# Kernel tuning notes

Hardware: AMD Instinct MI355X
Metric: run time of the kernel (lower is better)

The kernel has to match this reference:

```python
import jax, jax.numpy as jnp
import numpy as np

E = 8          # num_experts
D = 768        # d_model
H = 3072       # d_hidden
TOP_K = 2


def setup_inputs() -> dict:
    key = jax.random.key(0)
    ks = jax.random.split(key, 8)
    s_in = 1.0 / np.sqrt(D)
    s_h = 1.0 / np.sqrt(H)
    return {
        "hidden_states": jax.random.normal(ks[0], (2, 2048, D), dtype=jnp.float32),
        "gate_w": jax.random.normal(ks[1], (E, D), dtype=jnp.float32) * s_in,
        "gate_b": jnp.zeros((E,), dtype=jnp.float32),
        "w1": jax.random.normal(ks[2], (E, H, D), dtype=jnp.float32) * s_in,  # FMoELinear: [E, out, in]
        "b1": jnp.zeros((E, H), dtype=jnp.float32),
        "w2": jax.random.normal(ks[3], (E, D, H), dtype=jnp.float32) * s_h,
        "b2": jnp.zeros((E, D), dtype=jnp.float32),
        "bias": jnp.zeros((D,), dtype=jnp.float32),
    }


def reference(hidden_states, gate_w, gate_b, w1, b1, w2, b2, bias):
    B, S, d = hidden_states.shape
    x = hidden_states.reshape(-1, d)                      # [T, D]
    T = x.shape[0]
    # NaiveGate: linear gate, top-k, softmax over the top-k logits
    logits = x @ gate_w.T + gate_b                        # [T, E]
    top_val, top_idx = jax.lax.top_k(logits, TOP_K)       # [T, K]
    scores = jax.nn.softmax(top_val, axis=-1)             # [T, K]
    # combine weights: [T, E], score mass scattered to chosen experts
    combine = jnp.zeros((T, E), dtype=x.dtype)
    combine = combine.at[jnp.arange(T)[:, None], top_idx].add(scores)
    # expert MLPs (dense over experts, masked combine keeps routing math exact)
    h = jnp.einsum('td,ehd->teh', x, w1) + b1             # [T, E, H]
    h = jax.nn.gelu(h, approximate=False)                 # torch F.gelu (exact erf)
    y = jnp.einsum('teh,edh->ted', h, w2) + b2            # [T, E, D]
    out = jnp.einsum('te,ted->td', combine, y)            # [T, D]
    return out.reshape(B, S, d), bias
```

## Files before the change

### kernel.cpp

```cpp
#include <hip/hip_runtime.h>
#include <hip/hip_bf16.h>

#define DD 768
#define HH 3072
#define NE 8
#define TOPK 2

#define BK 64
#define CAP 1536
#define NRBMAX (CAP/128)
#define NB1 (HH / 128)
#define NB2 (DD / 128)

typedef __attribute__((ext_vector_type(8))) short short8;
typedef __attribute__((ext_vector_type(4))) float f32x4;

static __device__ __forceinline__ unsigned short f2bf(float v) {
    __hip_bfloat16 b = __float2bfloat16(v);
    return *reinterpret_cast<unsigned short*>(&b);
}

static __device__ __forceinline__ float gelu_f(float v) {
    float s = v * 0.70710678118f;
    float a = fabsf(s);
    float t = __builtin_amdgcn_rcpf(1.f + 0.3275911f * a);
    float poly = t * (0.254829592f + t * (-0.284496736f + t * (1.421413741f +
                 t * (-1.453152027f + t * 1.061405429f))));
    float erfv = 1.f - poly * __expf(-s * s);
    erfv = copysignf(erfv, s);
    return 0.5f * v * (1.f + erfv);
}

static __device__ __forceinline__ void cvt4(const float* __restrict__ src,
                                            unsigned short* __restrict__ dst, size_t j4)
{
    float4 v = *reinterpret_cast<const float4*>(&src[j4 * 4]);
    ushort4 o;
    o.x = f2bf(v.x); o.y = f2bf(v.y); o.z = f2bf(v.z); o.w = f2bf(v.w);
    *reinterpret_cast<ushort4*>(&dst[j4 * 4]) = o;
}

__global__ __launch_bounds__(256) void routecvt_kernel(
    const float* __restrict__ x, const float* __restrict__ gw, const float* __restrict__ gb,
    int* __restrict__ ctrl, int* __restrict__ pos_of, float* __restrict__ wpos,
    unsigned short* __restrict__ Xe, int T, int maxP,
    const float* __restrict__ w1, const float* __restrict__ w2,
    unsigned short* __restrict__ w1b, unsigned short* __restrict__ w2b, size_t nW4)
{
    __shared__ int s_e[32], s_rank[32];
    __shared__ float s_w[32];
    __shared__ int lh[NE], lbase[NE];

    int tid = threadIdx.x;
    int w = tid >> 6, lane = tid & 63;

    if ((int)blockIdx.x * 16 < T) {
        if (tid < NE) lh[tid] = 0;
        __syncthreads();

#pragma unroll
        for (int j = 0; j < 4; ++j) {
            int t = blockIdx.x * 16 + w * 4 + j;
            if (t >= T) break;
            float acc[NE];
#pragma unroll
            for (int e = 0; e < NE; ++e) acc[e] = 0.f;
            const float4* xr = reinterpret_cast<const float4*>(x + (size_t)t * DD);
#pragma unroll
            for (int k = 0; k < 3; ++k) {
                float4 xv = xr[k * 64 + lane];
#pragma unroll
                for (int e = 0; e < NE; ++e) {
                    float4 gv = *reinterpret_cast<const float4*>(&gw[e * DD + (k * 64 + lane) * 4]);
                    acc[e] += xv.x * gv.x + xv.y * gv.y + xv.z * gv.z + xv.w * gv.w;
                }
            }
#pragma unroll
            for (int e = 0; e < NE; ++e) {
                float v = acc[e];
                for (int off = 32; off; off >>= 1) v += __shfl_xor(v, off, 64);
                acc[e] = v;
            }
            if (lane == 0) {
                float lg[NE];
#pragma unroll
                for (int e = 0; e < NE; ++e) lg[e] = acc[e] + gb[e];
                int i0 = 0;
#pragma unroll
                for (int e = 1; e < NE; ++e) if (lg[e] > lg[i0]) i0 = e;
                int i1 = -1;
#pragma unroll
                for (int e = 0; e < NE; ++e) {
                    if (e == i0) continue;
                    if (i1 < 0 || lg[e] > lg[i1]) i1 = e;
                }
                float m = lg[i0];
                float e0 = __expf(lg[i0] - m), e1 = __expf(lg[i1] - m);
                float s = e0 + e1;
                int slot = (w * 4 + j) * 2;
                s_e[slot]     = i0; s_w[slot]     = e0 / s; s_rank[slot]     = atomicAdd(&lh[i0], 1);
                s_e[slot + 1] = i1; s_w[slot + 1] = e1 / s; s_rank[slot + 1] = atomicAdd(&lh[i1], 1);
            }
        }
        __syncthreads();

        if (tid < NE) lbase[tid] = lh[tid] ? atomicAdd(&ctrl[8 + tid], lh[tid]) : 0;
        __syncthreads();

#pragma unroll
        for (int j = 0; j < 4; ++j) {
            int t = blockIdx.x * 16 + w * 4 + j;
            if (t >= T) break;
            const float4* xr = reinterpret_cast<const float4*>(x + (size_t)t * DD);
            ushort4 o[3];
#pragma unroll
            for (int k = 0; k < 3; ++k) {
                float4 v = xr[k * 64 + lane];
                o[k].x = f2bf(v.x); o[k].y = f2bf(v.y); o[k].z = f2bf(v.z); o[k].w = f2bf(v.w);
            }
#pragma unroll
            for (int s = 0; s < 2; ++s) {
                int slot = (w * 4 + j) * 2 + s;
                int e = s_e[slot];
                int p = e * CAP + lbase[e] + s_rank[slot];
                p = min(p, maxP - 1);
                if (lane == 0) { pos_of[2 * t + s] = p; wpos[p] = s_w[slot]; }
#pragma unroll
                for (int k = 0; k < 3; ++k)
                    *reinterpret_cast<ushort4*>(&Xe[(size_t)p * DD + (k * 64 + lane) * 4]) = o[k];
            }
        }
    }

    size_t tot = 2 * nW4;
    for (size_t j = (size_t)blockIdx.x * 256 + tid; j < tot; j += (size_t)gridDim.x * 256) {
        if (j < nW4) cvt4(w1, w1b, j);
        else         cvt4(w2, w2b, j - nW4);
    }
}

static __device__ __forceinline__ void stage_tile(
    const unsigned short* __restrict__ g, int ld, unsigned short* __restrict__ lds)
{
    int tid = threadIdx.x;
#pragma unroll
    for (int r = 0; r < 4; ++r) {
        int j = (r << 8) + tid;
        int row = j >> 3;
        int kc = (j & 7) ^ (row & 7);
        __builtin_amdgcn_global_load_lds(
            (const __attribute__((address_space(1))) void*)(g + (size_t)row * ld + (kc << 3)),
            (__attribute__((address_space(3))) void*)(lds + (j << 3)),
            16, 0, 0);
    }
}

#define LDSF(base, row, kc) \
    reinterpret_cast<const short8*>(&(base)[((((row) << 3) + ((kc) ^ ((row) & 7))) << 3)])

static __device__ __forceinline__ void gemm_item(
    const unsigned short* __restrict__ Abase,
    const unsigned short* __restrict__ Bbase,
    int ld, int nt,
    unsigned short* __restrict__ As, unsigned short* __restrict__ Bs,
    f32x4 acc[4][4], int wr, int wc, int fr, int fq)
{
    const int BUF = 128 * 64;
    stage_tile(Abase, ld, As);
    stage_tile(Bbase, ld, Bs);
    for (int t = 0; t < nt; ++t) {
        int cur = t & 1;
        if (t + 1 < nt) {
            stage_tile(Abase + (size_t)(t + 1) * BK, ld, As + (cur ^ 1) * BUF);
            stage_tile(Bbase + (size_t)(t + 1) * BK, ld, Bs + (cur ^ 1) * BUF);
            asm volatile("s_waitcnt vmcnt(8)" ::: "memory");
        } else {
            asm volatile("s_waitcnt vmcnt(0)" ::: "memory");
        }
        __builtin_amdgcn_s_barrier();
        asm volatile("" ::: "memory");

        const unsigned short* A = As + cur * BUF;
        const unsigned short* B = Bs + cur * BUF;
        short8 a[2][4], b[2][4];
#pragma unroll
        for (int ks = 0; ks < 2; ++ks) {
            int kc = ks * 4 + fq;
#pragma unroll
            for (int m = 0; m < 4; ++m)
                a[ks][m] = *LDSF(A, wr + m * 16 + fr, kc);
#pragma unroll
            for (int n = 0; n < 4; ++n)
                b[ks][n] = *LDSF(B, wc + n * 16 + fr, kc);
        }
        __builtin_amdgcn_s_setprio(1);
#pragma unroll
        for (int ks = 0; ks < 2; ++ks)
#pragma unroll
            for (int m = 0; m < 4; ++m)
#pragma unroll
                for (int n = 0; n < 4; ++n)
                    acc[m][n] = __builtin_amdgcn_mfma_f32_16x16x32_bf16(
                        b[ks][n], a[ks][m], acc[m][n], 0, 0, 0);
        __builtin_amdgcn_s_setprio(0);
        asm volatile("s_waitcnt lgkmcnt(0)" ::: "memory");
        __builtin_amdgcn_s_barrier();
        asm volatile("" ::: "memory");
    }
}


__global__ __launch_bounds__(256, 2) void gemm1_kernel(
    const unsigned short* __restrict__ Xe, const unsigned short* __restrict__ W1b,
    const float* __restrict__ b1, unsigned short* __restrict__ H1,
    const int* __restrict__ ctrl, int* __restrict__ qcur)
{
    __shared__ unsigned short As[2 * 128 * 64];
    __shared__ unsigned short Bs[2 * 128 * 64];
    __shared__ int sh_item;
    __shared__ int nrbs[NE];
    __shared__ int tcum[192];

    int tid = threadIdx.x;
    if (tid < NE) {
        int cnt = ctrl[8 + tid];
        int nrb = (cnt + 127) >> 7;
        nrbs[tid] = nrb > NRBMAX ? NRBMAX : nrb;
    }
    __syncthreads();
    if (tid < 192) {
        int q = tid / 24, s0 = tid - q * 24;
        int c = 0;
        for (int i = 0; i <= s0; ++i) c += nrbs[(q + 8 * i) / NB1];
        tcum[tid] = c;
    }
    __syncthreads();

    int lane = tid & 63, w = tid >> 6;
    int wr = (w >> 1) * 64, wc = (w & 1) * 64;
    int fr = lane & 15, fq = lane >> 4;
    int q0 = blockIdx.x & 7;

    for (int off = 0; off < 8; ++off) {
        int qq = (q0 + off) & 7;
        int qtot = tcum[qq * 24 + 23];
        for (;;) {
            if (tid == 0) sh_item = atomicAdd(&qcur[qq * 16], 1);
            __syncthreads();
            int j = sh_item;
            __syncthreads();
            if (j >= qtot) break;

            int s = 0;
            while (tcum[qq * 24 + s] <= j) ++s;
            int pair = qq + 8 * s;
            int start = s ? tcum[qq * 24 + s - 1] : 0;
            int rb = j - start;
            int e = pair / NB1, cb = pair - e * NB1;
            int rowbase = e * CAP + (rb << 7);
            int colbase = cb << 7;

            const unsigned short* Abase = Xe + (size_t)rowbase * DD;
            const unsigned short* Bbase = W1b + (size_t)e * HH * DD + (size_t)colbase * DD;

            f32x4 acc[4][4];
#pragma unroll
            for (int m = 0; m < 4; ++m)
#pragma unroll
                for (int n = 0; n < 4; ++n) acc[m][n] = (f32x4){0.f, 0.f, 0.f, 0.f};

            gemm_item(Abase, Bbase, DD, DD / BK, As, Bs, acc, wr, wc, fr, fq);

            float4 bb[4];
#pragma unroll
            for (int n = 0; n < 4; ++n)
                bb[n] = *reinterpret_cast<const float4*>(
                    &b1[e * HH + colbase + wc + n * 16 + fq * 4]);
#pragma unroll
            for (int m = 0; m < 4; ++m) {
                int tok = rowbase + wr + m * 16 + fr;
#pragma unroll
                for (int n = 0; n < 4; ++n) {
                    int ch = colbase + wc + n * 16 + fq * 4;
                    ushort4 o;
                    o.x = f2bf(gelu_f(acc[m][n][0] + bb[n].x));
                    o.y = f2bf(gelu_f(acc[m][n][1] + bb[n].y));
                    o.z = f2bf(gelu_f(acc[m][n][2] + bb[n].z));
                    o.w = f2bf(gelu_f(acc[m][n][3] + bb[n].w));
                    *reinterpret_cast<ushort4*>(&H1[(size_t)tok * HH + ch]) = o;
                }
            }
        }
    }
}

__global__ __launch_bounds__(256, 2) void gemm2_kernel(
    const unsigned short* __restrict__ H1, const unsigned short* __restrict__ W2b,
    const float* __restrict__ b2, const float* __restrict__ wpos,
    float* __restrict__ Yb, const int* __restrict__ ctrl, int* __restrict__ qcur)
{
    __shared__ unsigned short As[2 * 128 * 64];
    __shared__ unsigned short Bs[2 * 128 * 64];
    __shared__ int sh_item;
    __shared__ int nrbs[NE];
    __shared__ int tcum[48];

    int tid = threadIdx.x;
    if (tid < NE) {
        int cnt = ctrl[8 + tid];
        int nrb = (cnt + 127) >> 7;
        nrbs[tid] = nrb > NRBMAX ? NRBMAX : nrb;
    }
    __syncthreads();
    if (tid < 48) {
        int q = tid / 6, s0 = tid - q * 6;
        int c = 0;
        for (int i = 0; i <= s0; ++i) c += nrbs[(q + 8 * i) / NB2];
        tcum[tid] = c;
    }
    __syncthreads();

    int lane = tid & 63, w = tid >> 6;
    int wr = (w >> 1) * 64, wc = (w & 1) * 64;
    int fr = lane & 15, fq = lane >> 4;
    int q0 = blockIdx.x & 7;

    for (int off = 0; off < 8; ++off) {
        int qq = (q0 + off) & 7;
        int qtot = tcum[qq * 6 + 5];
        for (;;) {
            if (tid == 0) sh_item = atomicAdd(&qcur[(8 + qq) * 16], 1);
            __syncthreads();
            int j = sh_item;
            __syncthreads();
            if (j >= qtot) break;

            int s = 0;
            while (tcum[qq * 6 + s] <= j) ++s;
            int g = qq + 8 * s;
            int start = s ? tcum[qq * 6 + s - 1] : 0;
            int rb = j - start;
            int e = g / NB2, cb = g - e * NB2;
            int rowbase = e * CAP + (rb << 7);
            int colbase = cb << 7;

            const unsigned short* Abase = H1 + (size_t)rowbase * HH;
            const unsigned short* Bbase = W2b + (size_t)e * DD * HH + (size_t)colbase * HH;

            f32x4 acc[4][4];
#pragma unroll
            for (int m = 0; m < 4; ++m)
#pragma unroll
                for (int n = 0; n < 4; ++n) acc[m][n] = (f32x4){0.f, 0.f, 0.f, 0.f};

            gemm_item(Abase, Bbase, HH, HH / BK, As, Bs, acc, wr, wc, fr, fq);

            float4 bb[4];
#pragma unroll
            for (int n = 0; n < 4; ++n)
                bb[n] = *reinterpret_cast<const float4*>(
                    &b2[e * DD + colbase + wc + n * 16 + fq * 4]);
#pragma unroll
            for (int m = 0; m < 4; ++m) {
                int tok = rowbase + wr + m * 16 + fr;
                float wp = wpos[tok];
#pragma unroll
                for (int n = 0; n < 4; ++n) {
                    int ch = colbase + wc + n * 16 + fq * 4;
                    float4 o;
                    o.x = wp * (acc[m][n][0] + bb[n].x);
                    o.y = wp * (acc[m][n][1] + bb[n].y);
                    o.z = wp * (acc[m][n][2] + bb[n].z);
                    o.w = wp * (acc[m][n][3] + bb[n].w);
                    *reinterpret_cast<float4*>(&Yb[(size_t)tok * DD + ch]) = o;
                }
            }
        }
    }
}

__global__ __launch_bounds__(256) void combine_kernel(
    const float* __restrict__ Yb, const int* __restrict__ pos_of,
    const float* __restrict__ bias, float* __restrict__ out, int T)
{
    int i = blockIdx.x * blockDim.x + threadIdx.x;
    int total = T * (DD / 4);
    if (i < total) {
        int t = i / (DD / 4);
        int c = (i % (DD / 4)) * 4;
        int p0 = pos_of[2 * t], p1 = pos_of[2 * t + 1];
        float4 v0 = *reinterpret_cast<const float4*>(&Yb[(size_t)p0 * DD + c]);
        float4 v1 = *reinterpret_cast<const float4*>(&Yb[(size_t)p1 * DD + c]);
        float4 o;
        o.x = v0.x + v1.x; o.y = v0.y + v1.y;
        o.z = v0.z + v1.z; o.w = v0.w + v1.w;
        *reinterpret_cast<float4*>(&out[(size_t)t * DD + c]) = o;
    } else if (i < total + DD / 4) {
        int c = (i - total) * 4;
        *reinterpret_cast<float4*>(&out[(size_t)T * DD + c]) =
            *reinterpret_cast<const float4*>(&bias[c]);
    }
}

extern "C" void kernel_launch(void* const* d_in, const int* in_sizes, int n_in,
                              void* d_out, int out_size, void* d_ws, size_t ws_size,
                              hipStream_t stream)
{
    const float* x    = (const float*)d_in[0];
    const float* gw   = (const float*)d_in[1];
    const float* gb   = (const float*)d_in[2];
    const float* w1   = (const float*)d_in[3];
    const float* b1   = (const float*)d_in[4];
    const float* w2   = (const float*)d_in[5];
    const float* b2   = (const float*)d_in[6];
    const float* bias = (const float*)d_in[7];
    float* out = (float*)d_out;

    int T = in_sizes[0] / DD;
    int nA = T * TOPK;
    int maxP = NE * CAP + 256;

    char* ws = (char*)d_ws;
    size_t off = 0;
    auto alloc = [&](size_t bytes) -> char* {
        char* p = ws + off;
        off += (bytes + 255) & ~(size_t)255;
        return p;
    };
    unsigned short* w1b = (unsigned short*)alloc((size_t)NE * HH * DD * 2);
    unsigned short* w2b = (unsigned short*)alloc((size_t)NE * DD * HH * 2);
    unsigned short* Xe  = (unsigned short*)alloc((size_t)maxP * DD * 2);
    unsigned short* H1  = (unsigned short*)alloc((size_t)maxP * HH * 2);
    float*  Yb          = (float*)alloc((size_t)maxP * DD * 4);
    int*    pos_of      = (int*)alloc((size_t)nA * 4);
    float*  wpos        = (float*)alloc((size_t)maxP * 4);
    int*    ctrl        = (int*)alloc(64 * 4);
    int*    qcur        = (int*)alloc(256 * 4);

    size_t nW = (size_t)NE * HH * DD;
    size_t nW4 = nW / 4;

    hipMemsetAsync(ctrl, 0, (64 + 256) * 4, stream);

    hipLaunchKernelGGL(routecvt_kernel, dim3(2048), dim3(256), 0, stream,
                       x, gw, gb, ctrl, pos_of, wpos, Xe, T, maxP,
                       w1, w2, w1b, w2b, nW4);
    hipLaunchKernelGGL(gemm1_kernel, dim3(512), dim3(256), 0, stream,
                       Xe, w1b, b1, H1, ctrl, qcur);
    hipLaunchKernelGGL(gemm2_kernel, dim3(512), dim3(256), 0, stream,
                       H1, w2b, b2, wpos, Yb, ctrl, qcur);
    hipLaunchKernelGGL(combine_kernel, dim3((T * (DD / 4) + DD / 4 + 255) / 256, 1, 1), dim3(256), 0, stream,
                       Yb, pos_of, bias, out, T);
}
```

Measured before the change: 210.5 us.

## Fuse top-k combine into gemm2 epilogue via atomic adds to output

Removes the intermediate Yb buffer and the separate combine kernel by having gemm2 scatter weighted expert outputs directly into the output with float atomicAdd, using a per-slot token index map. The output is zeroed with a memset, and the bias row copy moves into an idle routecvt block. Padding rows beyond each expert's count are skipped. This trades a kernel launch and a large fp32 round trip for many scalar atomic operations and nondeterministic summation order.

```diff
diff --git a/kernel.cpp b/kernel.cpp
--- a/kernel.cpp
+++ b/kernel.cpp
@@ -42,10 +42,11 @@
 
 __global__ __launch_bounds__(256) void routecvt_kernel(
     const float* __restrict__ x, const float* __restrict__ gw, const float* __restrict__ gb,
-    int* __restrict__ ctrl, int* __restrict__ pos_of, float* __restrict__ wpos,
+    int* __restrict__ ctrl, int* __restrict__ tok_of, float* __restrict__ wpos,
     unsigned short* __restrict__ Xe, int T, int maxP,
     const float* __restrict__ w1, const float* __restrict__ w2,
-    unsigned short* __restrict__ w1b, unsigned short* __restrict__ w2b, size_t nW4)
+    unsigned short* __restrict__ w1b, unsigned short* __restrict__ w2b, size_t nW4,
+    const float* __restrict__ bias, float* __restrict__ out)
 {
     __shared__ int s_e[32], s_rank[32];
     __shared__ float s_w[32];
@@ -124,12 +125,16 @@
                 int e = s_e[slot];
                 int p = e * CAP + lbase[e] + s_rank[slot];
                 p = min(p, maxP - 1);
-                if (lane == 0) { pos_of[2 * t + s] = p; wpos[p] = s_w[slot]; }
+                if (lane == 0) { tok_of[p] = t; wpos[p] = s_w[slot]; }
 #pragma unroll
                 for (int k = 0; k < 3; ++k)
                     *reinterpret_cast<ushort4*>(&Xe[(size_t)p * DD + (k * 64 + lane) * 4]) = o[k];
             }
         }
+    } else if (blockIdx.x == gridDim.x - 1) {
+        if (tid < DD / 4)
+            *reinterpret_cast<float4*>(&out[(size_t)T * DD + tid * 4]) =
+                *reinterpret_cast<const float4*>(&bias[tid * 4]);
     }
 
     size_t tot = 2 * nW4;
@@ -297,17 +302,19 @@
 __global__ __launch_bounds__(256, 2) void gemm2_kernel(
     const unsigned short* __restrict__ H1, const unsigned short* __restrict__ W2b,
     const float* __restrict__ b2, const float* __restrict__ wpos,
-    float* __restrict__ Yb, const int* __restrict__ ctrl, int* __restrict__ qcur)
+    const int* __restrict__ tok_of, float* __restrict__ out,
+    const int* __restrict__ ctrl, int* __restrict__ qcur)
 {
     __shared__ unsigned short As[2 * 128 * 64];
     __shared__ unsigned short Bs[2 * 128 * 64];
     __shared__ int sh_item;
-    __shared__ int nrbs[NE];
+    __shared__ int nrbs[NE], cnts[NE];
     __shared__ int tcum[48];
 
     int tid = threadIdx.x;
     if (tid < NE) {
         int cnt = ctrl[8 + tid];
+        cnts[tid] = cnt;
         int nrb = (cnt + 127) >> 7;
         nrbs[tid] = nrb > NRBMAX ? NRBMAX : nrb;
     }
@@ -360,45 +367,24 @@
             for (int n = 0; n < 4; ++n)
                 bb[n] = *reinterpret_cast<const float4*>(
                     &b2[e * DD + colbase + wc + n * 16 + fq * 4]);
+            int cnt_e = cnts[e];
 #pragma unroll
             for (int m = 0; m < 4; ++m) {
-                int tok = rowbase + wr + m * 16 + fr;
-                float wp = wpos[tok];
+                int p = rowbase + wr + m * 16 + fr;
+                if (p - e * CAP >= cnt_e) continue;
+                int t = tok_of[p];
+                float wp = wpos[p];
+                float* orow = &out[(size_t)t * DD];
 #pragma unroll
                 for (int n = 0; n < 4; ++n) {
                     int ch = colbase + wc + n * 16 + fq * 4;
-                    float4 o;
-                    o.x = wp * (acc[m][n][0] + bb[n].x);
-                    o.y = wp * (acc[m][n][1] + bb[n].y);
-                    o.z = wp * (acc[m][n][2] + bb[n].z);
-                    o.w = wp * (acc[m][n][3] + bb[n].w);
-                    *reinterpret_cast<float4*>(&Yb[(size_t)tok * DD + ch]) = o;
+                    atomicAdd(&orow[ch + 0], wp * (acc[m][n][0] + bb[n].x));
+                    atomicAdd(&orow[ch + 1], wp * (acc[m][n][1] + bb[n].y));
+                    atomicAdd(&orow[ch + 2], wp * (acc[m][n][2] + bb[n].z));
+                    atomicAdd(&orow[ch + 3], wp * (acc[m][n][3] + bb[n].w));
                 }
             }
         }
-    }
-}
-
-__global__ __launch_bounds__(256) void combine_kernel(
-    const float* __restrict__ Yb, const int* __restrict__ pos_of,
-    const float* __restrict__ bias, float* __restrict__ out, int T)
-{
-    int i = blockIdx.x * blockDim.x + threadIdx.x;
-    int total = T * (DD / 4);
-    if (i < total) {
-        int t = i / (DD / 4);
-        int c = (i % (DD / 4)) * 4;
-        int p0 = pos_of[2 * t], p1 = pos_of[2 * t + 1];
-        float4 v0 = *reinterpret_cast<const float4*>(&Yb[(size_t)p0 * DD + c]);
-        float4 v1 = *reinterpret_cast<const float4*>(&Yb[(size_t)p1 * DD + c]);
-        float4 o;
-        o.x = v0.x + v1.x; o.y = v0.y + v1.y;
-        o.z = v0.z + v1.z; o.w = v0.w + v1.w;
-        *reinterpret_cast<float4*>(&out[(size_t)t * DD + c]) = o;
-    } else if (i < total + DD / 4) {
-        int c = (i - total) * 4;
-        *reinterpret_cast<float4*>(&out[(size_t)T * DD + c]) =
-            *reinterpret_cast<const float4*>(&bias[c]);
     }
 }
 
@@ -417,7 +403,6 @@
     float* out = (float*)d_out;
 
     int T = in_sizes[0] / DD;
-    int nA = T * TOPK;
     int maxP = NE * CAP + 256;
 
     char* ws = (char*)d_ws;
@@ -431,8 +416,7 @@
     unsigned short* w2b = (unsigned short*)alloc((size_t)NE * DD * HH * 2);
     unsigned short* Xe  = (unsigned short*)alloc((size_t)maxP * DD * 2);
     unsigned short* H1  = (unsigned short*)alloc((size_t)maxP * HH * 2);
-    float*  Yb          = (float*)alloc((size_t)maxP * DD * 4);
-    int*    pos_of      = (int*)alloc((size_t)nA * 4);
+    int*    tok_of      = (int*)alloc((size_t)maxP * 4);
     float*  wpos        = (float*)alloc((size_t)maxP * 4);
     int*    ctrl        = (int*)alloc(64 * 4);
     int*    qcur        = (int*)alloc(256 * 4);
@@ -441,14 +425,13 @@
     size_t nW4 = nW / 4;
 
     hipMemsetAsync(ctrl, 0, (64 + 256) * 4, stream);
+    hipMemsetAsync(out, 0, ((size_t)T * DD) * 4, stream);
 
     hipLaunchKernelGGL(routecvt_kernel, dim3(2048), dim3(256), 0, stream,
-                       x, gw, gb, ctrl, pos_of, wpos, Xe, T, maxP,
-                       w1, w2, w1b, w2b, nW4);
+                       x, gw, gb, ctrl, tok_of, wpos, Xe, T, maxP,
+                       w1, w2, w1b, w2b, nW4, bias, out);
     hipLaunchKernelGGL(gemm1_kernel, dim3(512), dim3(256), 0, stream,
                        Xe, w1b, b1, H1, ctrl, qcur);
     hipLaunchKernelGGL(gemm2_kernel, dim3(512), dim3(256), 0, stream,
-                       H1, w2b, b2, wpos, Yb, ctrl, qcur);
-    hipLaunchKernelGGL(combine_kernel, dim3((T * (DD / 4) + DD / 4 + 255) / 256, 1, 1), dim3(256), 0, stream,
-                       Yb, pos_of, bias, out, T);
-}
+                       H1, w2b, b2, wpos, tok_of, out, ctrl, qcur);
+}
```

Result: slower. 280.8 us (+33.4%).
